# Optimization experiments

Measured on AMD Instinct MI355X. Metric: run time of the kernel, lower is better.

## Reference

```python
import jax, jax.numpy as jnp
import numpy as np

NUM_HEAD = 8
KEY_DIM = 256   # total key dim
VALUE_DIM = 256 # total value dim
OUT_DIM = 256
B, Q, K = 128, 384, 384


def setup_inputs() -> dict:
    key = jax.random.key(0)
    ks = jax.random.split(key, 11)
    hk = KEY_DIM // NUM_HEAD   # per-head key dim = 32
    hv = VALUE_DIM // NUM_HEAD # per-head value dim = 32
    s = 0.02
    return {
        "q_data": jax.random.normal(ks[0], (B, Q, KEY_DIM), jnp.float32),
        "m_data": jax.random.normal(ks[1], (B, K, VALUE_DIM), jnp.float32),
        "bias": jax.random.normal(ks[2], (B, 1, Q, K), jnp.float32),
        "nonbatched_bias": jax.random.normal(ks[3], (NUM_HEAD, Q, K), jnp.float32),
        "q_weights": jax.random.normal(ks[4], (KEY_DIM, NUM_HEAD, hk), jnp.float32) * s,
        "k_weights": jax.random.normal(ks[5], (VALUE_DIM, NUM_HEAD, hk), jnp.float32) * s,
        "v_weights": jax.random.normal(ks[6], (VALUE_DIM, NUM_HEAD, hv), jnp.float32) * s,
        "o_weights": jax.random.normal(ks[7], (NUM_HEAD, hv, OUT_DIM), jnp.float32) * s,
        "o_bias": jax.random.normal(ks[8], (OUT_DIM,), jnp.float32) * s,
        "gating_w": jax.random.normal(ks[9], (KEY_DIM, NUM_HEAD, hv), jnp.float32) * s,
        "gating_b": jnp.ones((NUM_HEAD, hv), jnp.float32),
    }


def reference(q_data, m_data, bias, nonbatched_bias,
              q_weights, k_weights, v_weights, o_weights, o_bias,
              gating_w, gating_b):
    hk = q_weights.shape[-1]
    scale = hk ** (-0.5)
    q = jnp.einsum('bqa,ahc->bqhc', q_data, q_weights) * scale
    k = jnp.einsum('bka,ahc->bkhc', m_data, k_weights)
    v = jnp.einsum('bka,ahc->bkhc', m_data, v_weights)
    # logits: [b,h,q,k] with additive pair bias and per-head nonbatched bias
    logits = jnp.einsum('bqhc,bkhc->bhqk', q, k) + bias + nonbatched_bias[None]
    weights = jax.nn.softmax(logits, axis=-1)
    weighted_avg = jnp.einsum('bhqk,bkhc->bqhc', weights, v)
    gate = jax.nn.sigmoid(jnp.einsum('bqc,chv->bqhv', q_data, gating_w) + gating_b)
    weighted_avg = weighted_avg * gate
    return jnp.einsum('bqhc,hco->bqo', weighted_avg, o_weights) + o_bias
```

## Files before the change

kernel.cpp:

```cpp
#include <hip/hip_runtime.h>
#include <hip/hip_bf16.h>

#define DM 256
#define NB 128
#define SQ 384
#define SK 384

typedef __bf16 bf16x4 __attribute__((ext_vector_type(4)));
typedef __bf16 bf16x8 __attribute__((ext_vector_type(8)));
typedef float f32x4 __attribute__((ext_vector_type(4)));
typedef unsigned short u16;
typedef unsigned int u32;

union BF8 { bf16x8 v8; bf16x4 v4[2]; uint2 u2[2]; };

__device__ __forceinline__ u16 f2bf(float f) {
    union { float fv; u32 u; } v; v.fv = f;
    u32 r = v.u + 0x7FFFu + ((v.u >> 16) & 1u);
    return (u16)(r >> 16);
}
__device__ __forceinline__ float bf2f(u16 u) {
    union { u32 v; float f; } x; x.v = ((u32)u) << 16; return x.f;
}
__device__ __forceinline__ uint2 pack4(float a, float b, float c, float d) {
    uint2 r;
    r.x = (u32)f2bf(a) | ((u32)f2bf(b) << 16);
    r.y = (u32)f2bf(c) | ((u32)f2bf(d) << 16);
    return r;
}
__device__ __forceinline__ uint2 pack4c(f32x4 v) {
    bf16x4 t;
    t[0] = (__bf16)v[0]; t[1] = (__bf16)v[1];
    t[2] = (__bf16)v[2]; t[3] = (__bf16)v[3];
    union { bf16x4 b; uint2 u; } cv; cv.b = t; return cv.u;
}
__device__ __forceinline__ void glds16(const void* g, void* l) {
    __builtin_amdgcn_global_load_lds(
        (const __attribute__((address_space(1))) unsigned int*)g,
        (__attribute__((address_space(3))) unsigned int*)l, 16, 0, 0);
}

__global__ __launch_bounds__(256)
void prep_w(const float* __restrict__ q_w, const float* __restrict__ k_w,
            const float* __restrict__ v_w, const float* __restrict__ g_w,
            const float* __restrict__ o_w, u16* __restrict__ wt)
{
    __shared__ float t[64][65];
    const int mat = blockIdx.z;
    const float* src = mat == 0 ? q_w : mat == 1 ? k_w : mat == 2 ? v_w : mat == 3 ? g_w : o_w;
    const float scale = (mat == 0) ? (float)(0.17677669529663687 * 1.4426950408889634) : 1.0f;
    const int k0 = blockIdx.x * 64, n0 = blockIdx.y * 64;
    const int tid = threadIdx.x;
#pragma unroll
    for (int i = 0; i < 4; ++i) {
        int pos = tid + i * 256;
        int r = pos >> 4, c4 = (pos & 15) * 4;
        f32x4 v = *(const f32x4*)&src[(size_t)(k0 + r) * DM + n0 + c4];
        t[r][c4 + 0] = v[0]; t[r][c4 + 1] = v[1]; t[r][c4 + 2] = v[2]; t[r][c4 + 3] = v[3];
    }
    __syncthreads();
    const int nr = tid >> 2, kq = (tid & 3) * 16;
    u16* dst = wt + (size_t)mat * DM * DM + (size_t)(n0 + nr) * DM + k0 + kq;
#pragma unroll
    for (int j = 0; j < 16; j += 4) {
        uint2 p = pack4(t[kq + j][nr] * scale, t[kq + j + 1][nr] * scale,
                        t[kq + j + 2][nr] * scale, t[kq + j + 3][nr] * scale);
        *(uint2*)&dst[j] = p;
    }
}

__global__ __launch_bounds__(256)
void prep_nb(const float* __restrict__ nb, float* __restrict__ nb2)
{
    int i = (blockIdx.x * 256 + threadIdx.x) * 4;
    f32x4 v = *(const f32x4*)&nb[i];
    *(f32x4*)&nb2[i] = v * 1.4426950408889634f - 20.0f;
}

template<int MODE>
__global__ __launch_bounds__(256)
void proj_kernel(const float* __restrict__ Af, const u16* __restrict__ Abf,
                 const u16* __restrict__ Wt1, const u16* __restrict__ Wt2,
                 const float* __restrict__ gb, const float* __restrict__ ob,
                 u16* __restrict__ out1, u16* __restrict__ gate,
                 u16* __restrict__ vT, float* __restrict__ outf)
{
    __shared__ u16 Wlds[64 * 256];
    const int tid = threadIdx.x, lane = tid & 63, w = tid >> 6;
    const int lr = lane & 15, lg = lane >> 4;
    const int m0 = blockIdx.x * 128;

    BF8 af0[8], af1[8];
    if (MODE <= 1) {
        const float* ar0 = Af + (size_t)(m0 + w * 16 + lr) * DM + 4 * lg;
        const float* ar1 = ar0 + (size_t)64 * DM;
#pragma unroll
        for (int ks = 0; ks < 8; ++ks) {
            f32x4 v0 = *(const f32x4*)&ar0[ks * 32];
            f32x4 v1 = *(const f32x4*)&ar0[ks * 32 + 16];
            af0[ks].u2[0] = pack4(v0[0], v0[1], v0[2], v0[3]);
            af0[ks].u2[1] = pack4(v1[0], v1[1], v1[2], v1[3]);
            f32x4 w0 = *(const f32x4*)&ar1[ks * 32];
            f32x4 w1 = *(const f32x4*)&ar1[ks * 32 + 16];
            af1[ks].u2[0] = pack4(w0[0], w0[1], w0[2], w0[3]);
            af1[ks].u2[1] = pack4(w1[0], w1[1], w1[2], w1[3]);
        }
    } else {
        const u16* ar0 = Abf + (size_t)(m0 + w * 16 + lr) * DM + 4 * lg;
        const u16* ar1 = ar0 + (size_t)64 * DM;
#pragma unroll
        for (int ks = 0; ks < 8; ++ks) {
            af0[ks].u2[0] = *(const uint2*)&ar0[ks * 32];
            af0[ks].u2[1] = *(const uint2*)&ar0[ks * 32 + 16];
            af1[ks].u2[0] = *(const uint2*)&ar1[ks * 32];
            af1[ks].u2[1] = *(const uint2*)&ar1[ks * 32 + 16];
        }
    }

    const int NSLAB = (MODE == 2) ? 4 : 8;
    for (int sl = 0; sl < NSLAB; ++sl) {
        const u16* Wsrc = (sl < 4) ? Wt1 : Wt2;
        const int n0 = (sl & 3) * 64;
        if (sl) __syncthreads();
#pragma unroll
        for (int i = 0; i < 8; ++i) {
            int pos = tid + i * 256;
            int nr = pos >> 5, c8 = (pos & 31) * 8;
            uint4 gv = *(const uint4*)&Wsrc[(size_t)(n0 + nr) * DM + c8];
            int within = c8 & 31;
            int pa2 = (c8 >> 5) * 64 + ((within >> 3) & 1) * 32 + (within >> 4) * 8;
            int sw = (nr & 7) << 4;
            char* rb_ = (char*)Wlds + nr * 512;
            *(uint2*)(rb_ + (pa2 ^ sw)) = make_uint2(gv.x, gv.y);
            *(uint2*)(rb_ + ((pa2 + 16) ^ sw)) = make_uint2(gv.z, gv.w);
        }
        __syncthreads();

        f32x4 acc0[4], acc1[4];
#pragma unroll
        for (int nf = 0; nf < 4; ++nf) {
            acc0[nf] = (f32x4){0.f, 0.f, 0.f, 0.f};
            acc1[nf] = (f32x4){0.f, 0.f, 0.f, 0.f};
        }
#pragma unroll
        for (int ks = 0; ks < 8; ++ks) {
#pragma unroll
            for (int nf = 0; nf < 4; ++nf) {
                int row = nf * 16 + lr;
                bf16x8 bfr = *(const bf16x8*)((char*)Wlds + row * 512 +
                                              ((ks * 64 + lg * 16) ^ ((row & 7) << 4)));
                acc0[nf] = __builtin_amdgcn_mfma_f32_16x16x32_bf16(af0[ks].v8, bfr, acc0[nf], 0, 0, 0);
                acc1[nf] = __builtin_amdgcn_mfma_f32_16x16x32_bf16(af1[ks].v8, bfr, acc1[nf], 0, 0, 0);
            }
        }

#pragma unroll
        for (int rg = 0; rg < 2; ++rg) {
            const int mb = m0 + rg * 64;
#pragma unroll
            for (int nf = 0; nf < 4; ++nf) {
                f32x4 accv = rg ? acc1[nf] : acc0[nf];
                int n = n0 + nf * 16 + lr;
                int gn = (sl & 3) * 64 + nf * 16 + lr;
                if (MODE == 0) {
                    if (sl < 4) {
#pragma unroll
                        for (int r = 0; r < 4; ++r)
                            out1[(size_t)(mb + w * 16 + 4 * lg + r) * DM + n] = f2bf(accv[r]);
                    } else {
                        float gbv = gb[gn];
#pragma unroll
                        for (int r = 0; r < 4; ++r)
                            gate[(size_t)(mb + w * 16 + 4 * lg + r) * DM + gn] =
                                f2bf(1.f / (1.f + __expf(-(accv[r] + gbv))));
                    }
                } else if (MODE == 1) {
                    if (sl < 4) {
                        int pn = (n & ~31) | (((n >> 2) & 3) << 3) | (((n >> 4) & 1) << 2) | (n & 3);
#pragma unroll
                        for (int r = 0; r < 4; ++r)
                            out1[(size_t)(mb + w * 16 + 4 * lg + r) * DM + pn] = f2bf(accv[r]);
                    } else {
                        int bb = mb / SQ;
                        int kkl = mb - bb * SQ + w * 16 + 4 * lg;
                        int cc = kkl & 31;
                        int kkp = (kkl & ~31) | (((cc >> 2) & 3) << 3) | (((cc >> 4) & 1) << 2);
                        *(uint2*)&vT[(size_t)(bb * DM + gn) * SK + kkp] =
                            pack4(accv[0], accv[1], accv[2], accv[3]);
                    }
                } else {
                    float obv = ob[n];
#pragma unroll
                    for (int r = 0; r < 4; ++r)
                        outf[(size_t)(mb + w * 16 + 4 * lg + r) * DM + n] = accv[r] + obv;
                }
            }
        }
    }
}

__global__ __launch_bounds__(256, 1)
void attn_kernel(const u16* __restrict__ Qb, const u16* __restrict__ Kb,
                 const u16* __restrict__ vT, const u16* __restrict__ gateb,
                 const float* __restrict__ bias, const float* __restrict__ nb2,
                 u16* __restrict__ wavg)
{
    extern __shared__ char smem[];
    const int tid = threadIdx.x, lane = tid & 63, hw = tid >> 6;
    const int lr = lane & 15, lg = lane >> 4;
    const int bid = blockIdx.x;
    const int pair = bid >> 1, hg = bid & 1;
    const int qt = pair >> 7, b = pair & 127;
    const int q0 = qt * 64;
    const int h = hg * 4 + hw;
    const float LOG2E = 1.4426950408889634f;

    const int ciA = hw * 64 + lane, ciB = 256 + hw * 64 + lane;
    const int krA = ciA >> 4, kjA = (ciA & 15) ^ (krA & 7);
    const int krB = ciB >> 4, kjB = (ciB & 15) ^ (krB & 7);
    const u16* kgA = Kb + ((size_t)b * SK + krA) * DM + hg * 128 + kjA * 8;
    const u16* kgB = Kb + ((size_t)b * SK + krB) * DM + hg * 128 + kjB * 8;
    const int vrA = ciA >> 2, vjA = (ciA & 3) ^ ((vrA >> 1) & 3);
    const int vrB = ciB >> 2, vjB = (ciB & 3) ^ ((vrB >> 1) & 3);
    const u16* vgA = vT + ((size_t)b * DM + hg * 128 + vrA) * SK + vjA * 8;
    const u16* vgB = vT + ((size_t)b * DM + hg * 128 + vrB) * SK + vjB * 8;
    const int bqA = ciA >> 3, bjA = (ciA & 7) ^ (bqA & 7);
    const int bqB = ciB >> 3, bjB = (ciB & 7) ^ (bqB & 7);
    const float* bgA = bias + ((size_t)b * SQ + q0 + bqA) * SK + bjA * 4;
    const float* bgB = bias + ((size_t)b * SQ + q0 + bqB) * SK + bjB * 4;

    const int dA = hw * 1024, dB = 4096 + hw * 1024;

    BF8 qf[4];
    {
        const u16* qp = Qb + (size_t)(b * SQ + q0 + lr) * DM + h * 32 + 4 * lg;
#pragma unroll
        for (int nf = 0; nf < 4; ++nf) {
            qf[nf].u2[0] = *(const uint2*)&qp[nf * 16 * DM];
            qf[nf].u2[1] = *(const uint2*)&qp[nf * 16 * DM + 16];
        }
    }

    f32x4 Oacc[2][4];
    float lsum[4];
#pragma unroll
    for (int nf = 0; nf < 4; ++nf) {
        lsum[nf] = 0.f;
        Oacc[0][nf] = (f32x4){0.f, 0.f, 0.f, 0.f};
        Oacc[1][nf] = (f32x4){0.f, 0.f, 0.f, 0.f};
    }

    const float* np = nb2 + ((size_t)h * SQ + q0) * SK + 4 * lg;

    auto stage = [&](char* buf) {
        glds16(kgA, buf + dA); glds16(kgB, buf + dB);
        glds16(vgA, buf + 8192 + dA); glds16(vgB, buf + 8192 + dB);
        glds16(bgA, buf + 16384 + dA); glds16(bgB, buf + 16384 + dB);
        kgA += 32 * DM; kgB += 32 * DM; vgA += 32; vgB += 32; bgA += 32; bgB += 32;
    };

    stage(smem);
    asm volatile("s_waitcnt vmcnt(0)" ::: "memory");
    __builtin_amdgcn_s_barrier();

    int cur = 0;
#pragma unroll 1
    for (int kb = 0; kb < 12; ++kb) {
        const int k0 = kb * 32;
        char* buf = smem + cur * 24576;
        char* Kc = buf; char* Vc = buf + 8192; char* Bc = buf + 16384;

        f32x4 n4r[4][2];
#pragma unroll
        for (int nf = 0; nf < 4; ++nf)
#pragma unroll
            for (int rb = 0; rb < 2; ++rb)
                n4r[nf][rb] = *(const f32x4*)&np[(size_t)(nf * 16 + lr) * SK + k0 + rb * 16];
        __builtin_amdgcn_sched_barrier(0);

        if (kb < 11) stage(smem + (cur ^ 1) * 24576);

        f32x4 st[4][2];
        __builtin_amdgcn_s_setprio(1);
#pragma unroll
        for (int nf = 0; nf < 4; ++nf)
#pragma unroll
            for (int rb = 0; rb < 2; ++rb) {
                bf16x8 kfr = *(const bf16x8*)(Kc + (rb * 16 + lr) * 256 +
                                              (((hw * 4 + lg) ^ (lr & 7)) << 4));
                st[nf][rb] = __builtin_amdgcn_mfma_f32_16x16x32_bf16(
                    kfr, qf[nf].v8, (f32x4){0.f, 0.f, 0.f, 0.f}, 0, 0, 0);
            }
        __builtin_amdgcn_s_setprio(0);

        BF8 pvv[4];
#pragma unroll
        for (int nf = 0; nf < 4; ++nf)
#pragma unroll
            for (int rb = 0; rb < 2; ++rb) {
                f32x4 b4 = *(const f32x4*)(Bc + (nf * 16 + lr) * 128 +
                                           (((rb * 4 + lg) ^ (lr & 7)) << 4));
                f32x4 s = st[nf][rb] + b4 * LOG2E + n4r[nf][rb];
                f32x4 e;
                e[0] = __builtin_amdgcn_exp2f(s[0]);
                e[1] = __builtin_amdgcn_exp2f(s[1]);
                e[2] = __builtin_amdgcn_exp2f(s[2]);
                e[3] = __builtin_amdgcn_exp2f(s[3]);
                lsum[nf] += (e[0] + e[1]) + (e[2] + e[3]);
                pvv[nf].u2[rb] = pack4c(e);
            }

        __builtin_amdgcn_s_setprio(1);
#pragma unroll
        for (int cf = 0; cf < 2; ++cf) {
            int row = hw * 32 + cf * 16 + lr;
            bf16x8 vfr = *(const bf16x8*)(Vc + row * 64 + ((lg ^ ((lr >> 1) & 3)) << 4));
#pragma unroll
            for (int nf = 0; nf < 4; ++nf)
                Oacc[cf][nf] = __builtin_amdgcn_mfma_f32_16x16x32_bf16(
                    vfr, pvv[nf].v8, Oacc[cf][nf], 0, 0, 0);
        }
        __builtin_amdgcn_s_setprio(0);

        if (kb < 11) {
            asm volatile("s_waitcnt vmcnt(0)" ::: "memory");
            __builtin_amdgcn_s_barrier();
            cur ^= 1;
        }
    }

#pragma unroll
    for (int nf = 0; nf < 4; ++nf) {
        lsum[nf] += __shfl_xor(lsum[nf], 16, 64);
        lsum[nf] += __shfl_xor(lsum[nf], 32, 64);
    }

#pragma unroll
    for (int nf = 0; nf < 4; ++nf) {
        float rl = 1.0f / lsum[nf];
        size_t qrow = (size_t)(b * SQ + q0 + nf * 16 + lr);
#pragma unroll
        for (int cf = 0; cf < 2; ++cf) {
            size_t idx = qrow * DM + h * 32 + cf * 16 + 4 * lg;
            uint2 g2 = *(const uint2*)&gateb[idx];
            float g0 = bf2f((u16)(g2.x & 0xffff)), g1 = bf2f((u16)(g2.x >> 16));
            float g2f = bf2f((u16)(g2.y & 0xffff)), g3 = bf2f((u16)(g2.y >> 16));
            f32x4 o = Oacc[cf][nf];
            *(uint2*)&wavg[idx] = pack4(o[0] * rl * g0, o[1] * rl * g1,
                                        o[2] * rl * g2f, o[3] * rl * g3);
        }
    }
}

extern "C" void kernel_launch(void* const* d_in, const int* in_sizes, int n_in,
                              void* d_out, int out_size, void* d_ws, size_t ws_size,
                              hipStream_t stream) {
    const float* q_data = (const float*)d_in[0];
    const float* m_data = (const float*)d_in[1];
    const float* bias   = (const float*)d_in[2];
    const float* nbias  = (const float*)d_in[3];
    const float* q_w    = (const float*)d_in[4];
    const float* k_w    = (const float*)d_in[5];
    const float* v_w    = (const float*)d_in[6];
    const float* o_w    = (const float*)d_in[7];
    const float* o_b    = (const float*)d_in[8];
    const float* g_w    = (const float*)d_in[9];
    const float* g_b    = (const float*)d_in[10];
    float* out = (float*)d_out;

    const size_t MB = (size_t)NB * SQ * DM * 2;
    char* ws = (char*)d_ws;
    u16* qb    = (u16*)(ws);
    u16* kb    = (u16*)(ws + MB);
    u16* vTb   = (u16*)(ws + 2 * MB);
    u16* gateb = (u16*)(ws + 3 * MB);
    u16* wavg  = (u16*)(ws + 4 * MB);
    u16* wt    = (u16*)(ws + 5 * MB);
    float* nb2 = (float*)(ws + 5 * MB + 655360);
    u16* Wtq = wt, *Wtk = wt + 65536, *Wtv = wt + 2 * 65536,
       *Wtg = wt + 3 * 65536, *Wto = wt + 4 * 65536;

    prep_w<<<dim3(4, 4, 5), 256, 0, stream>>>(q_w, k_w, v_w, g_w, o_w, wt);
    prep_nb<<<1152, 256, 0, stream>>>(nbias, nb2);
    proj_kernel<0><<<384, 256, 0, stream>>>(q_data, nullptr, Wtq, Wtg, g_b, nullptr,
                                            qb, gateb, nullptr, nullptr);
    proj_kernel<1><<<384, 256, 0, stream>>>(m_data, nullptr, Wtk, Wtv, nullptr, nullptr,
                                            kb, nullptr, vTb, nullptr);

    const int ATTN_SMEM = 2 * 24576;
    hipFuncSetAttribute((const void*)attn_kernel,
                        hipFuncAttributeMaxDynamicSharedMemorySize, ATTN_SMEM);
    attn_kernel<<<1536, 256, ATTN_SMEM, stream>>>(qb, kb, vTb, gateb, bias, nb2, wavg);

    proj_kernel<2><<<384, 256, 0, stream>>>(nullptr, wavg, Wto, nullptr, nullptr, o_b,
                                            nullptr, nullptr, nullptr, out);
}
```

Before: 251.2 us.

## Merge Q/gate, K/V projections and nb prep into one launch; remap attention blocks

Combines the bias-prep kernel and the two input-projection kernels into a single launch. Blocks are split by index ranges into Q/gate projection, K/V projection and nonbatched-bias scaling, which cuts launch overhead and the tail idle time between small kernels. The output projection moves into its own non-templated kernel. The attention kernel's block index is also remapped so that consecutive blocks are spread across batch/head pairs, likely aimed at better cache locality or balance across XCDs. In exchange the merged kernel uses a runtime mode branch, which may raise register pressure.

```diff
diff --git a/kernel.cpp b/kernel.cpp
--- a/kernel.cpp
+++ b/kernel.cpp
@@ -70,28 +70,37 @@
 }
 
 __global__ __launch_bounds__(256)
-void prep_nb(const float* __restrict__ nb, float* __restrict__ nb2)
+void proj01_kernel(const float* __restrict__ Aq, const float* __restrict__ Am,
+                   const u16* __restrict__ Wtq, const u16* __restrict__ Wtg,
+                   const u16* __restrict__ Wtk, const u16* __restrict__ Wtv,
+                   const float* __restrict__ gb, const float* __restrict__ nbias,
+                   u16* __restrict__ qb, u16* __restrict__ gateb,
+                   u16* __restrict__ kb, u16* __restrict__ vT,
+                   float* __restrict__ nb2)
 {
-    int i = (blockIdx.x * 256 + threadIdx.x) * 4;
-    f32x4 v = *(const f32x4*)&nb[i];
-    *(f32x4*)&nb2[i] = v * 1.4426950408889634f - 20.0f;
-}
-
-template<int MODE>
-__global__ __launch_bounds__(256)
-void proj_kernel(const float* __restrict__ Af, const u16* __restrict__ Abf,
-                 const u16* __restrict__ Wt1, const u16* __restrict__ Wt2,
-                 const float* __restrict__ gb, const float* __restrict__ ob,
-                 u16* __restrict__ out1, u16* __restrict__ gate,
-                 u16* __restrict__ vT, float* __restrict__ outf)
-{
+    const int bx = blockIdx.x;
+    const int tid = threadIdx.x;
+    if (bx >= 768) {
+        const size_t base = ((size_t)(bx - 768) * 256 + tid) * 16;
+#pragma unroll
+        for (int i = 0; i < 4; ++i) {
+            f32x4 v = *(const f32x4*)&nbias[base + i * 4];
+            *(f32x4*)&nb2[base + i * 4] = v * 1.4426950408889634f - 20.0f;
+        }
+        return;
+    }
+    const int mode = bx >= 384;
+    const int m0 = (mode ? bx - 384 : bx) * 128;
+    const float* Af = mode ? Am : Aq;
+    const u16* W1 = mode ? Wtk : Wtq;
+    const u16* W2 = mode ? Wtv : Wtg;
+
     __shared__ u16 Wlds[64 * 256];
-    const int tid = threadIdx.x, lane = tid & 63, w = tid >> 6;
+    const int lane = tid & 63, w = tid >> 6;
     const int lr = lane & 15, lg = lane >> 4;
-    const int m0 = blockIdx.x * 128;
 
     BF8 af0[8], af1[8];
-    if (MODE <= 1) {
+    {
         const float* ar0 = Af + (size_t)(m0 + w * 16 + lr) * DM + 4 * lg;
         const float* ar1 = ar0 + (size_t)64 * DM;
 #pragma unroll
@@ -105,21 +114,10 @@
             af1[ks].u2[0] = pack4(w0[0], w0[1], w0[2], w0[3]);
             af1[ks].u2[1] = pack4(w1[0], w1[1], w1[2], w1[3]);
         }
-    } else {
-        const u16* ar0 = Abf + (size_t)(m0 + w * 16 + lr) * DM + 4 * lg;
-        const u16* ar1 = ar0 + (size_t)64 * DM;
-#pragma unroll
-        for (int ks = 0; ks < 8; ++ks) {
-            af0[ks].u2[0] = *(const uint2*)&ar0[ks * 32];
-            af0[ks].u2[1] = *(const uint2*)&ar0[ks * 32 + 16];
-            af1[ks].u2[0] = *(const uint2*)&ar1[ks * 32];
-            af1[ks].u2[1] = *(const uint2*)&ar1[ks * 32 + 16];
-        }
-    }
-
-    const int NSLAB = (MODE == 2) ? 4 : 8;
-    for (int sl = 0; sl < NSLAB; ++sl) {
-        const u16* Wsrc = (sl < 4) ? Wt1 : Wt2;
+    }
+
+    for (int sl = 0; sl < 8; ++sl) {
+        const u16* Wsrc = (sl < 4) ? W1 : W2;
         const int n0 = (sl & 3) * 64;
         if (sl) __syncthreads();
 #pragma unroll
@@ -162,24 +160,24 @@
                 f32x4 accv = rg ? acc1[nf] : acc0[nf];
                 int n = n0 + nf * 16 + lr;
                 int gn = (sl & 3) * 64 + nf * 16 + lr;
-                if (MODE == 0) {
+                if (mode == 0) {
                     if (sl < 4) {
 #pragma unroll
                         for (int r = 0; r < 4; ++r)
-                            out1[(size_t)(mb + w * 16 + 4 * lg + r) * DM + n] = f2bf(accv[r]);
+                            qb[(size_t)(mb + w * 16 + 4 * lg + r) * DM + n] = f2bf(accv[r]);
                     } else {
                         float gbv = gb[gn];
 #pragma unroll
                         for (int r = 0; r < 4; ++r)
-                            gate[(size_t)(mb + w * 16 + 4 * lg + r) * DM + gn] =
+                            gateb[(size_t)(mb + w * 16 + 4 * lg + r) * DM + gn] =
                                 f2bf(1.f / (1.f + __expf(-(accv[r] + gbv))));
                     }
-                } else if (MODE == 1) {
+                } else {
                     if (sl < 4) {
                         int pn = (n & ~31) | (((n >> 2) & 3) << 3) | (((n >> 4) & 1) << 2) | (n & 3);
 #pragma unroll
                         for (int r = 0; r < 4; ++r)
-                            out1[(size_t)(mb + w * 16 + 4 * lg + r) * DM + pn] = f2bf(accv[r]);
+                            kb[(size_t)(mb + w * 16 + 4 * lg + r) * DM + pn] = f2bf(accv[r]);
                     } else {
                         int bb = mb / SQ;
                         int kkl = mb - bb * SQ + w * 16 + 4 * lg;
@@ -188,12 +186,80 @@
                         *(uint2*)&vT[(size_t)(bb * DM + gn) * SK + kkp] =
                             pack4(accv[0], accv[1], accv[2], accv[3]);
                     }
-                } else {
-                    float obv = ob[n];
-#pragma unroll
-                    for (int r = 0; r < 4; ++r)
-                        outf[(size_t)(mb + w * 16 + 4 * lg + r) * DM + n] = accv[r] + obv;
                 }
+            }
+        }
+    }
+}
+
+__global__ __launch_bounds__(256)
+void out_proj_kernel(const u16* __restrict__ Abf, const u16* __restrict__ Wto,
+                     const float* __restrict__ ob, float* __restrict__ outf)
+{
+    __shared__ u16 Wlds[64 * 256];
+    const int tid = threadIdx.x, lane = tid & 63, w = tid >> 6;
+    const int lr = lane & 15, lg = lane >> 4;
+    const int m0 = blockIdx.x * 128;
+
+    BF8 af0[8], af1[8];
+    {
+        const u16* ar0 = Abf + (size_t)(m0 + w * 16 + lr) * DM + 4 * lg;
+        const u16* ar1 = ar0 + (size_t)64 * DM;
+#pragma unroll
+        for (int ks = 0; ks < 8; ++ks) {
+            af0[ks].u2[0] = *(const uint2*)&ar0[ks * 32];
+            af0[ks].u2[1] = *(const uint2*)&ar0[ks * 32 + 16];
+            af1[ks].u2[0] = *(const uint2*)&ar1[ks * 32];
+            af1[ks].u2[1] = *(const uint2*)&ar1[ks * 32 + 16];
+        }
+    }
+
+    for (int sl = 0; sl < 4; ++sl) {
+        const int n0 = sl * 64;
+        if (sl) __syncthreads();
+#pragma unroll
+        for (int i = 0; i < 8; ++i) {
+            int pos = tid + i * 256;
+            int nr = pos >> 5, c8 = (pos & 31) * 8;
+            uint4 gv = *(const uint4*)&Wto[(size_t)(n0 + nr) * DM + c8];
+            int within = c8 & 31;
+            int pa2 = (c8 >> 5) * 64 + ((within >> 3) & 1) * 32 + (within >> 4) * 8;
+            int sw = (nr & 7) << 4;
+            char* rb_ = (char*)Wlds + nr * 512;
+            *(uint2*)(rb_ + (pa2 ^ sw)) = make_uint2(gv.x, gv.y);
+            *(uint2*)(rb_ + ((pa2 + 16) ^ sw)) = make_uint2(gv.z, gv.w);
+        }
+        __syncthreads();
+
+        f32x4 acc0[4], acc1[4];
+#pragma unroll
+        for (int nf = 0; nf < 4; ++nf) {
+            acc0[nf] = (f32x4){0.f, 0.f, 0.f, 0.f};
+            acc1[nf] = (f32x4){0.f, 0.f, 0.f, 0.f};
+        }
+#pragma unroll
+        for (int ks = 0; ks < 8; ++ks) {
+#pragma unroll
+            for (int nf = 0; nf < 4; ++nf) {
+                int row = nf * 16 + lr;
+                bf16x8 bfr = *(const bf16x8*)((char*)Wlds + row * 512 +
+                                              ((ks * 64 + lg * 16) ^ ((row & 7) << 4)));
+                acc0[nf] = __builtin_amdgcn_mfma_f32_16x16x32_bf16(af0[ks].v8, bfr, acc0[nf], 0, 0, 0);
+                acc1[nf] = __builtin_amdgcn_mfma_f32_16x16x32_bf16(af1[ks].v8, bfr, acc1[nf], 0, 0, 0);
+            }
+        }
+
+#pragma unroll
+        for (int rg = 0; rg < 2; ++rg) {
+            const int mb = m0 + rg * 64;
+#pragma unroll
+            for (int nf = 0; nf < 4; ++nf) {
+                f32x4 accv = rg ? acc1[nf] : acc0[nf];
+                int n = n0 + nf * 16 + lr;
+                float obv = ob[n];
+#pragma unroll
+                for (int r = 0; r < 4; ++r)
+                    outf[(size_t)(mb + w * 16 + 4 * lg + r) * DM + n] = accv[r] + obv;
             }
         }
     }
@@ -208,7 +274,8 @@
     extern __shared__ char smem[];
     const int tid = threadIdx.x, lane = tid & 63, hw = tid >> 6;
     const int lr = lane & 15, lg = lane >> 4;
-    const int bid = blockIdx.x;
+    const int bid0 = blockIdx.x;
+    const int bid = (bid0 & 7) * 192 + (bid0 >> 3);
     const int pair = bid >> 1, hg = bid & 1;
     const int qt = pair >> 7, b = pair & 127;
     const int q0 = qt * 64;
@@ -381,17 +448,13 @@
        *Wtg = wt + 3 * 65536, *Wto = wt + 4 * 65536;
 
     prep_w<<<dim3(4, 4, 5), 256, 0, stream>>>(q_w, k_w, v_w, g_w, o_w, wt);
-    prep_nb<<<1152, 256, 0, stream>>>(nbias, nb2);
-    proj_kernel<0><<<384, 256, 0, stream>>>(q_data, nullptr, Wtq, Wtg, g_b, nullptr,
-                                            qb, gateb, nullptr, nullptr);
-    proj_kernel<1><<<384, 256, 0, stream>>>(m_data, nullptr, Wtk, Wtv, nullptr, nullptr,
-                                            kb, nullptr, vTb, nullptr);
+    proj01_kernel<<<1056, 256, 0, stream>>>(q_data, m_data, Wtq, Wtg, Wtk, Wtv,
+                                            g_b, nbias, qb, gateb, kb, vTb, nb2);
 
     const int ATTN_SMEM = 2 * 24576;
     hipFuncSetAttribute((const void*)attn_kernel,
                         hipFuncAttributeMaxDynamicSharedMemorySize, ATTN_SMEM);
     attn_kernel<<<1536, 256, ATTN_SMEM, stream>>>(qb, kb, vTb, gateb, bias, nb2, wavg);
 
-    proj_kernel<2><<<384, 256, 0, stream>>>(nullptr, wavg, Wto, nullptr, nullptr, o_b,
-                                            nullptr, nullptr, nullptr, out);
-}
+    out_proj_kernel<<<384, 256, 0, stream>>>(wavg, Wto, o_b, out);
+}
```

Measured after the change: 232.8 us, median of 2. -7.3%, faster.
